# Optimization experiments

Hardware: AMD Instinct MI355X
Metric: run time of the kernel (lower is better)

The kernel has to match this reference:

```python
import jax, jax.numpy as jnp
import numpy as np

N_NODES = 100000
N_EDGES = 800000
IN_DIM = 128
HID = 128


def setup_inputs() -> dict:
    key = jax.random.key(0)
    ks = jax.random.split(key, 8)
    s = 0.05
    x = jax.random.normal(ks[0], (N_NODES, IN_DIM), jnp.float32)
    edge_index = jax.random.randint(ks[1], (2, N_EDGES), 0, N_NODES)
    return {
        "x": x,
        "edge_index": edge_index,
        "W1l": jax.random.normal(ks[2], (HID, IN_DIM), jnp.float32) * s,
        "b1l": jnp.zeros((HID,), jnp.float32),
        "W1r": jax.random.normal(ks[3], (HID, IN_DIM), jnp.float32) * s,
        "W2l": jax.random.normal(ks[4], (HID, HID), jnp.float32) * s,
        "b2l": jnp.zeros((HID,), jnp.float32),
        "W2r": jax.random.normal(ks[5], (HID, HID), jnp.float32) * s,
        "Wm1": jax.random.normal(ks[6], (HID, 2 * HID), jnp.float32) * s,
        "bm1": jnp.zeros((HID,), jnp.float32),
        "Wm2": jax.random.normal(ks[7], (1, HID), jnp.float32) * s,
        "bm2": jnp.zeros((1,), jnp.float32),
    }


def sage_conv(x, src, dst, Wl, bl, Wr):
    # PyG SAGEConv (mean aggr): out = lin_l(mean_{j in N(i)} x_j) + lin_r(x_i)
    msg = x[src]  # [E, d] gather of source features
    agg = jax.ops.segment_sum(msg, dst, num_segments=N_NODES)  # [N, d]
    deg = jax.ops.segment_sum(jnp.ones((src.shape[0],), x.dtype), dst, num_segments=N_NODES)
    agg = agg / jnp.maximum(deg, 1.0)[:, None]
    return agg @ Wl.T + bl + x @ Wr.T


def reference(x, edge_index, W1l, b1l, W1r, W2l, b2l, W2r, Wm1, bm1, Wm2, bm2):
    src, dst = edge_index[0], edge_index[1]
    h = jax.nn.relu(sage_conv(x, src, dst, W1l, b1l, W1r))  # dropout = identity (eval)
    h = jax.nn.relu(sage_conv(h, src, dst, W2l, b2l, W2r))
    ef = jnp.concatenate([h[src], h[dst]], axis=1)  # [E, 2*HID]
    hidden = jax.nn.relu(ef @ Wm1.T + bm1)  # [E, HID]
    logits = (hidden @ Wm2.T + bm2)[:, 0]  # [E]
    return jax.nn.sigmoid(logits)
```

## Files before the change

kernel.cpp:

```cpp
#include <hip/hip_runtime.h>
#include <math.h>

#define NN 100000
#define NE 800000
#define D 128

typedef __attribute__((ext_vector_type(8))) short bf16x8;
typedef __attribute__((ext_vector_type(8))) unsigned short u16x8;
typedef __attribute__((ext_vector_type(4))) float f32x4;
typedef __attribute__((ext_vector_type(2))) float f32x2;

constexpr size_t OFF_RS  = 0;
constexpr size_t OFF_CNT = 512 * 1024;
constexpr size_t OFF_CUR = 1024 * 1024;
constexpr size_t OFF_BS  = 1536 * 1024;
constexpr size_t OFF_WB  = 1552 * 1024;
constexpr size_t OFF_SRC = 2 * 1024 * 1024;
constexpr size_t OFF_EID = 6 * 1024 * 1024;
constexpr size_t OFF_V8  = 10 * 1024 * 1024;
constexpr size_t OFF_X8  = OFF_V8 + 13 * 1024 * 1024;
constexpr size_t OFF_H8  = OFF_X8 + 13 * 1024 * 1024;
constexpr size_t OFF_U8  = OFF_H8 + 13 * 1024 * 1024;

__device__ __forceinline__ unsigned short f2b(float f) {
    unsigned u = __builtin_bit_cast(unsigned, f);
    return (unsigned short)((u + 0x7FFFu + ((u >> 16) & 1u)) >> 16);
}
__device__ __forceinline__ float b2f(unsigned short h) {
    unsigned u = ((unsigned)h) << 16;
    return __builtin_bit_cast(float, u);
}

__global__ __launch_bounds__(256) void k_prep(const float* __restrict__ x,
                                              unsigned* __restrict__ x8w,
                                              const float* __restrict__ W1l,
                                              const float* __restrict__ W1r,
                                              const float* __restrict__ W2l,
                                              const float* __restrict__ W2r,
                                              const float* __restrict__ Wm1,
                                              unsigned short* __restrict__ wb,
                                              const int* __restrict__ dst,
                                              int* __restrict__ cnt) {
    int bid = blockIdx.x, tid = threadIdx.x;
    if (bid < 12500) {
        int i = bid * 256 + tid;
        float4 v = *(const float4*)&x[(size_t)i * 4];
        unsigned p = __builtin_amdgcn_cvt_pk_fp8_f32(v.x, v.y, 0u, false);
        p = __builtin_amdgcn_cvt_pk_fp8_f32(v.z, v.w, p, true);
        x8w[i] = p;
    } else if (bid < 12884) {
        int i = (bid - 12500) * 256 + tid;
        float v;
        if (i < 16384) v = W1l[i];
        else if (i < 32768) v = W1r[i - 16384];
        else if (i < 49152) v = W2l[i - 32768];
        else if (i < 65536) v = W2r[i - 49152];
        else v = Wm1[i - 65536];
        wb[i] = f2b(v);
    } else {
        int e = (bid - 12884) * 256 + tid;
        atomicAdd(&cnt[dst[e]], 1);
    }
}

__global__ __launch_bounds__(256) void k_scan1(const int* __restrict__ cnt,
                                               int* __restrict__ bsum) {
    int i = blockIdx.x * 256 + threadIdx.x;
    int v = (i < NN) ? cnt[i] : 0;
    #pragma unroll
    for (int o = 1; o < 64; o <<= 1) v += __shfl_xor(v, o);
    __shared__ int wsum[4];
    if ((threadIdx.x & 63) == 0) wsum[threadIdx.x >> 6] = v;
    __syncthreads();
    if (threadIdx.x == 0) bsum[blockIdx.x] = wsum[0] + wsum[1] + wsum[2] + wsum[3];
}

__global__ __launch_bounds__(512) void k_scan2(int* __restrict__ bsum, int nb) {
    __shared__ int s[512];
    int t = threadIdx.x;
    int v = (t < nb) ? bsum[t] : 0;
    s[t] = v;
    __syncthreads();
    for (int o = 1; o < 512; o <<= 1) {
        int u = (t >= o) ? s[t - o] : 0;
        __syncthreads();
        s[t] += u;
        __syncthreads();
    }
    if (t < nb) bsum[t] = s[t] - v;
}

__global__ __launch_bounds__(256) void k_scan3(const int* __restrict__ cnt,
                                               const int* __restrict__ bsum,
                                               int* __restrict__ rs,
                                               int* __restrict__ cur) {
    __shared__ int s[256];
    int t = threadIdx.x;
    int i = blockIdx.x * 256 + t;
    int v = (i < NN) ? cnt[i] : 0;
    s[t] = v;
    __syncthreads();
    for (int o = 1; o < 256; o <<= 1) {
        int u = (t >= o) ? s[t - o] : 0;
        __syncthreads();
        s[t] += u;
        __syncthreads();
    }
    int ex = s[t] - v + bsum[blockIdx.x];
    if (i < NN) { rs[i] = ex; cur[i] = ex; }
    if (i == NN - 1) rs[NN] = ex + v;
}

__global__ __launch_bounds__(256) void k_scatter_idx(const int* __restrict__ src,
                                                     const int* __restrict__ dst,
                                                     int* __restrict__ cur,
                                                     int* __restrict__ srcs,
                                                     int* __restrict__ eids) {
    int e = blockIdx.x * 256 + threadIdx.x;
    if (e < NE) {
        int pos = atomicAdd(&cur[dst[e]], 1);
        srcs[pos] = src[e];
        eids[pos] = e;
    }
}

#define UNPK8(acc, u) {                                               \
    f32x2 p0 = __builtin_amdgcn_cvt_pk_f32_fp8(u.x, false);           \
    f32x2 p1 = __builtin_amdgcn_cvt_pk_f32_fp8(u.x, true);            \
    f32x2 p2 = __builtin_amdgcn_cvt_pk_f32_fp8(u.y, false);           \
    f32x2 p3 = __builtin_amdgcn_cvt_pk_f32_fp8(u.y, true);            \
    acc[0] += p0.x; acc[1] += p0.y; acc[2] += p1.x; acc[3] += p1.y;   \
    acc[4] += p2.x; acc[5] += p2.y; acc[6] += p3.x; acc[7] += p3.y; }

__device__ __forceinline__ void gather_mean64(const unsigned char* __restrict__ feat8,
                                              const int* __restrict__ rs,
                                              const int* __restrict__ re,
                                              const int* __restrict__ srcs,
                                              int n0, unsigned short* agt) {
    const int tid = threadIdx.x;
    const int g = tid >> 4, q = tid & 15;
    #pragma unroll
    for (int half = 0; half < 2; ++half) {
        int r = half * 32 + g;
        int n = n0 + r;
        if (n > NN - 1) n = NN - 1;
        int b = rs[n], e = re[n];
        float a0[8] = {}, a1[8] = {}, a2[8] = {}, a3[8] = {};
        int j = b;
        for (; j + 7 < e; j += 8) {
            uint2 v0 = *(const uint2*)&feat8[(size_t)srcs[j]     * 128 + q * 8];
            uint2 v1 = *(const uint2*)&feat8[(size_t)srcs[j + 1] * 128 + q * 8];
            uint2 v2 = *(const uint2*)&feat8[(size_t)srcs[j + 2] * 128 + q * 8];
            uint2 v3 = *(const uint2*)&feat8[(size_t)srcs[j + 3] * 128 + q * 8];
            uint2 v4 = *(const uint2*)&feat8[(size_t)srcs[j + 4] * 128 + q * 8];
            uint2 v5 = *(const uint2*)&feat8[(size_t)srcs[j + 5] * 128 + q * 8];
            uint2 v6 = *(const uint2*)&feat8[(size_t)srcs[j + 6] * 128 + q * 8];
            uint2 v7 = *(const uint2*)&feat8[(size_t)srcs[j + 7] * 128 + q * 8];
            UNPK8(a0, v0); UNPK8(a1, v1); UNPK8(a2, v2); UNPK8(a3, v3);
            UNPK8(a0, v4); UNPK8(a1, v5); UNPK8(a2, v6); UNPK8(a3, v7);
        }
        for (; j + 3 < e; j += 4) {
            uint2 v0 = *(const uint2*)&feat8[(size_t)srcs[j]     * 128 + q * 8];
            uint2 v1 = *(const uint2*)&feat8[(size_t)srcs[j + 1] * 128 + q * 8];
            uint2 v2 = *(const uint2*)&feat8[(size_t)srcs[j + 2] * 128 + q * 8];
            uint2 v3 = *(const uint2*)&feat8[(size_t)srcs[j + 3] * 128 + q * 8];
            UNPK8(a0, v0); UNPK8(a1, v1); UNPK8(a2, v2); UNPK8(a3, v3);
        }
        for (; j < e; ++j) {
            uint2 v0 = *(const uint2*)&feat8[(size_t)srcs[j] * 128 + q * 8];
            UNPK8(a0, v0);
        }
        float inv = 1.0f / fmaxf((float)(e - b), 1.0f);
        u16x8 o;
        #pragma unroll
        for (int i = 0; i < 8; ++i) o[i] = f2b((a0[i] + a1[i] + a2[i] + a3[i]) * inv);
        *(u16x8*)&agt[r * 136 + q * 8] = o;
    }
}

__device__ __forceinline__ void stage_tile_fp8in(const unsigned char* __restrict__ src8,
                                                 int n0, unsigned short* t) {
    const int tid = threadIdx.x;
    int r = tid >> 3, q = tid & 7;
    int gr = n0 + r;
    if (gr > NN - 1) gr = NN - 1;
    uint4 v = *(const uint4*)&src8[(size_t)gr * 128 + q * 16];
    u16x8 o0, o1;
    f32x2 p;
    p = __builtin_amdgcn_cvt_pk_f32_fp8(v.x, false); o0[0] = f2b(p.x); o0[1] = f2b(p.y);
    p = __builtin_amdgcn_cvt_pk_f32_fp8(v.x, true);  o0[2] = f2b(p.x); o0[3] = f2b(p.y);
    p = __builtin_amdgcn_cvt_pk_f32_fp8(v.y, false); o0[4] = f2b(p.x); o0[5] = f2b(p.y);
    p = __builtin_amdgcn_cvt_pk_f32_fp8(v.y, true);  o0[6] = f2b(p.x); o0[7] = f2b(p.y);
    p = __builtin_amdgcn_cvt_pk_f32_fp8(v.z, false); o1[0] = f2b(p.x); o1[1] = f2b(p.y);
    p = __builtin_amdgcn_cvt_pk_f32_fp8(v.z, true);  o1[2] = f2b(p.x); o1[3] = f2b(p.y);
    p = __builtin_amdgcn_cvt_pk_f32_fp8(v.w, false); o1[4] = f2b(p.x); o1[5] = f2b(p.y);
    p = __builtin_amdgcn_cvt_pk_f32_fp8(v.w, true);  o1[6] = f2b(p.x); o1[7] = f2b(p.y);
    *(u16x8*)&t[r * 136 + q * 16]     = o0;
    *(u16x8*)&t[r * 136 + q * 16 + 8] = o1;
}

__device__ __forceinline__ void store_tile_fp8(const unsigned short* t,
                                               int n0, unsigned char* __restrict__ dst8) {
    const int tid = threadIdx.x;
    #pragma unroll
    for (int it = 0; it < 4; ++it) {
        int w = it * 512 + tid;
        int r = w >> 5, c4 = (w & 31) * 4;
        int gr = n0 + r;
        if (gr < NN) {
            unsigned p = __builtin_amdgcn_cvt_pk_fp8_f32(
                b2f(t[r * 136 + c4 + 0]), b2f(t[r * 136 + c4 + 1]), 0u, false);
            p = __builtin_amdgcn_cvt_pk_fp8_f32(
                b2f(t[r * 136 + c4 + 2]), b2f(t[r * 136 + c4 + 3]), p, true);
            *(unsigned*)&dst8[(size_t)gr * 128 + c4] = p;
        }
    }
}

__global__ __launch_bounds__(512) void k_aggconv1(const unsigned char* __restrict__ x8,
                                                  const int* __restrict__ rs,
                                                  const int* __restrict__ re,
                                                  const int* __restrict__ srcs,
                                                  const unsigned short* __restrict__ Wlb,
                                                  const unsigned short* __restrict__ Wrb,
                                                  const float* __restrict__ bias,
                                                  unsigned char* __restrict__ h8) {
    __shared__ unsigned short agt[64 * 136];
    __shared__ unsigned short sto[64 * 136];
    const int tid = threadIdx.x;
    const int n0 = blockIdx.x * 64;

    stage_tile_fp8in(x8, n0, sto);
    gather_mean64(x8, rs, re, srcs, n0, agt);
    __syncthreads();

    const int wv = tid >> 6, l = tid & 63;
    const int lrow = l & 15, lk = (l >> 4) * 8;
    f32x4 acc[4] = {};
    #pragma unroll
    for (int p = 0; p < 2; ++p) {
        const unsigned short* W  = p ? Wrb : Wlb;
        const unsigned short* At = p ? sto : agt;
        #pragma unroll
        for (int ks = 0; ks < 4; ++ks) {
            bf16x8 bfr = *(const bf16x8*)&W[(size_t)(wv * 16 + lrow) * D + ks * 32 + lk];
            #pragma unroll
            for (int mt = 0; mt < 4; ++mt) {
                bf16x8 af = *(const bf16x8*)&At[(mt * 16 + lrow) * 136 + ks * 32 + lk];
                acc[mt] = __builtin_amdgcn_mfma_f32_16x16x32_bf16(af, bfr, acc[mt], 0, 0, 0);
            }
        }
    }
    __syncthreads();
    const int orow = (l >> 4) * 4, ocol = l & 15;
    float bb = bias[wv * 16 + ocol];
    #pragma unroll
    for (int mt = 0; mt < 4; ++mt)
        #pragma unroll
        for (int j = 0; j < 4; ++j)
            sto[(mt * 16 + orow + j) * 136 + wv * 16 + ocol] =
                f2b(fmaxf(acc[mt][j] + bb, 0.0f));
    __syncthreads();
    store_tile_fp8(sto, n0, h8);
}

__global__ __launch_bounds__(512) void k_aggconv2uv(const unsigned char* __restrict__ h8,
                                                    const int* __restrict__ rs,
                                                    const int* __restrict__ re,
                                                    const int* __restrict__ srcs,
                                                    const unsigned short* __restrict__ Wlb,
                                                    const unsigned short* __restrict__ Wrb,
                                                    const float* __restrict__ bias,
                                                    const unsigned short* __restrict__ Wm1b,
                                                    const float* __restrict__ bm1,
                                                    unsigned char* __restrict__ U8,
                                                    unsigned char* __restrict__ V8) {
    __shared__ unsigned short agt[64 * 136];
    __shared__ unsigned short sto[64 * 136];
    const int tid = threadIdx.x;
    const int n0 = blockIdx.x * 64;

    stage_tile_fp8in(h8, n0, sto);
    gather_mean64(h8, rs, re, srcs, n0, agt);
    __syncthreads();

    const int wv = tid >> 6, l = tid & 63;
    const int lrow = l & 15, lk = (l >> 4) * 8;
    const int orow = (l >> 4) * 4, ocol = l & 15;

    f32x4 acc[4] = {};
    #pragma unroll
    for (int p = 0; p < 2; ++p) {
        const unsigned short* W  = p ? Wrb : Wlb;
        const unsigned short* At = p ? sto : agt;
        #pragma unroll
        for (int ks = 0; ks < 4; ++ks) {
            bf16x8 bfr = *(const bf16x8*)&W[(size_t)(wv * 16 + lrow) * D + ks * 32 + lk];
            #pragma unroll
            for (int mt = 0; mt < 4; ++mt) {
                bf16x8 af = *(const bf16x8*)&At[(mt * 16 + lrow) * 136 + ks * 32 + lk];
                acc[mt] = __builtin_amdgcn_mfma_f32_16x16x32_bf16(af, bfr, acc[mt], 0, 0, 0);
            }
        }
    }
    __syncthreads();
    {
        float bb = bias[wv * 16 + ocol];
        #pragma unroll
        for (int mt = 0; mt < 4; ++mt)
            #pragma unroll
            for (int j = 0; j < 4; ++j)
                agt[(mt * 16 + orow + j) * 136 + wv * 16 + ocol] =
                    f2b(fmaxf(acc[mt][j] + bb, 0.0f));
    }
    __syncthreads();

    f32x4 aU[4] = {}, aV[4] = {};
    #pragma unroll
    for (int ks = 0; ks < 4; ++ks) {
        bf16x8 bu = *(const bf16x8*)&Wm1b[(size_t)(wv * 16 + lrow) * 256 + ks * 32 + lk];
        bf16x8 bv = *(const bf16x8*)&Wm1b[(size_t)(wv * 16 + lrow) * 256 + 128 + ks * 32 + lk];
        #pragma unroll
        for (int mt = 0; mt < 4; ++mt) {
            bf16x8 af = *(const bf16x8*)&agt[(mt * 16 + lrow) * 136 + ks * 32 + lk];
            aU[mt] = __builtin_amdgcn_mfma_f32_16x16x32_bf16(af, bu, aU[mt], 0, 0, 0);
            aV[mt] = __builtin_amdgcn_mfma_f32_16x16x32_bf16(af, bv, aV[mt], 0, 0, 0);
        }
    }
    {
        float bb = bm1[wv * 16 + ocol];
        #pragma unroll
        for (int mt = 0; mt < 4; ++mt)
            #pragma unroll
            for (int j = 0; j < 4; ++j)
                sto[(mt * 16 + orow + j) * 136 + wv * 16 + ocol] = f2b(aU[mt][j] + bb);
    }
    __syncthreads();
    store_tile_fp8(sto, n0, U8);
    {
        #pragma unroll
        for (int mt = 0; mt < 4; ++mt)
            #pragma unroll
            for (int j = 0; j < 4; ++j)
                agt[(mt * 16 + orow + j) * 136 + wv * 16 + ocol] = f2b(aV[mt][j]);
    }
    __syncthreads();
    store_tile_fp8(agt, n0, V8);
}

__global__ __launch_bounds__(256) void k_edge2(const unsigned char* __restrict__ U8,
                                               const unsigned char* __restrict__ V8,
                                               const int* __restrict__ rs,
                                               const int* __restrict__ re,
                                               const int* __restrict__ srcs,
                                               const int* __restrict__ eids,
                                               const float* __restrict__ wm2,
                                               const float* __restrict__ bm2,
                                               float* __restrict__ out) {
    int t = blockIdx.x * 256 + threadIdx.x;
    int g = t >> 4, q = t & 15;
    if (g >= NN) return;
    int b = rs[g], e = re[g];
    if (b == e) return;
    uint2 vv = *(const uint2*)&V8[(size_t)g * 128 + q * 8];
    float vf[8], wf[8];
    {
        f32x2 p0 = __builtin_amdgcn_cvt_pk_f32_fp8(vv.x, false);
        f32x2 p1 = __builtin_amdgcn_cvt_pk_f32_fp8(vv.x, true);
        f32x2 p2 = __builtin_amdgcn_cvt_pk_f32_fp8(vv.y, false);
        f32x2 p3 = __builtin_amdgcn_cvt_pk_f32_fp8(vv.y, true);
        vf[0] = p0.x; vf[1] = p0.y; vf[2] = p1.x; vf[3] = p1.y;
        vf[4] = p2.x; vf[5] = p2.y; vf[6] = p3.x; vf[7] = p3.y;
    }
    float4 w0 = *(const float4*)&wm2[q * 8];
    float4 w1 = *(const float4*)&wm2[q * 8 + 4];
    wf[0] = w0.x; wf[1] = w0.y; wf[2] = w0.z; wf[3] = w0.w;
    wf[4] = w1.x; wf[5] = w1.y; wf[6] = w1.z; wf[7] = w1.w;
    const float bb = bm2[0];

#define EDOT(p, u) {                                                   \
    f32x2 q0 = __builtin_amdgcn_cvt_pk_f32_fp8(u.x, false);            \
    f32x2 q1 = __builtin_amdgcn_cvt_pk_f32_fp8(u.x, true);             \
    f32x2 q2 = __builtin_amdgcn_cvt_pk_f32_fp8(u.y, false);            \
    f32x2 q3 = __builtin_amdgcn_cvt_pk_f32_fp8(u.y, true);             \
    p += fmaxf(q0.x + vf[0], 0.0f) * wf[0] + fmaxf(q0.y + vf[1], 0.0f) * wf[1] \
       + fmaxf(q1.x + vf[2], 0.0f) * wf[2] + fmaxf(q1.y + vf[3], 0.0f) * wf[3] \
       + fmaxf(q2.x + vf[4], 0.0f) * wf[4] + fmaxf(q2.y + vf[5], 0.0f) * wf[5] \
       + fmaxf(q3.x + vf[6], 0.0f) * wf[6] + fmaxf(q3.y + vf[7], 0.0f) * wf[7]; }

    int j = b;
    for (; j + 7 < e; j += 8) {
        uint2 u0 = *(const uint2*)&U8[(size_t)srcs[j]     * 128 + q * 8];
        uint2 u1 = *(const uint2*)&U8[(size_t)srcs[j + 1] * 128 + q * 8];
        uint2 u2 = *(const uint2*)&U8[(size_t)srcs[j + 2] * 128 + q * 8];
        uint2 u3 = *(const uint2*)&U8[(size_t)srcs[j + 3] * 128 + q * 8];
        uint2 u4 = *(const uint2*)&U8[(size_t)srcs[j + 4] * 128 + q * 8];
        uint2 u5 = *(const uint2*)&U8[(size_t)srcs[j + 5] * 128 + q * 8];
        uint2 u6 = *(const uint2*)&U8[(size_t)srcs[j + 6] * 128 + q * 8];
        uint2 u7 = *(const uint2*)&U8[(size_t)srcs[j + 7] * 128 + q * 8];
        float p0 = 0.f, p1 = 0.f, p2 = 0.f, p3 = 0.f;
        float p4 = 0.f, p5 = 0.f, p6 = 0.f, p7 = 0.f;
        EDOT(p0, u0); EDOT(p1, u1); EDOT(p2, u2); EDOT(p3, u3);
        EDOT(p4, u4); EDOT(p5, u5); EDOT(p6, u6); EDOT(p7, u7);
        #pragma unroll
        for (int off = 1; off < 16; off <<= 1) {
            p0 += __shfl_xor(p0, off); p1 += __shfl_xor(p1, off);
            p2 += __shfl_xor(p2, off); p3 += __shfl_xor(p3, off);
            p4 += __shfl_xor(p4, off); p5 += __shfl_xor(p5, off);
            p6 += __shfl_xor(p6, off); p7 += __shfl_xor(p7, off);
        }
        if (q == 0) {
            out[eids[j]]     = 1.0f / (1.0f + expf(-(p0 + bb)));
            out[eids[j + 1]] = 1.0f / (1.0f + expf(-(p1 + bb)));
            out[eids[j + 2]] = 1.0f / (1.0f + expf(-(p2 + bb)));
            out[eids[j + 3]] = 1.0f / (1.0f + expf(-(p3 + bb)));
            out[eids[j + 4]] = 1.0f / (1.0f + expf(-(p4 + bb)));
            out[eids[j + 5]] = 1.0f / (1.0f + expf(-(p5 + bb)));
            out[eids[j + 6]] = 1.0f / (1.0f + expf(-(p6 + bb)));
            out[eids[j + 7]] = 1.0f / (1.0f + expf(-(p7 + bb)));
        }
    }
    for (; j + 3 < e; j += 4) {
        uint2 u0 = *(const uint2*)&U8[(size_t)srcs[j]     * 128 + q * 8];
        uint2 u1 = *(const uint2*)&U8[(size_t)srcs[j + 1] * 128 + q * 8];
        uint2 u2 = *(const uint2*)&U8[(size_t)srcs[j + 2] * 128 + q * 8];
        uint2 u3 = *(const uint2*)&U8[(size_t)srcs[j + 3] * 128 + q * 8];
        float p0 = 0.f, p1 = 0.f, p2 = 0.f, p3 = 0.f;
        EDOT(p0, u0); EDOT(p1, u1); EDOT(p2, u2); EDOT(p3, u3);
        #pragma unroll
        for (int off = 1; off < 16; off <<= 1) {
            p0 += __shfl_xor(p0, off); p1 += __shfl_xor(p1, off);
            p2 += __shfl_xor(p2, off); p3 += __shfl_xor(p3, off);
        }
        if (q == 0) {
            out[eids[j]]     = 1.0f / (1.0f + expf(-(p0 + bb)));
            out[eids[j + 1]] = 1.0f / (1.0f + expf(-(p1 + bb)));
            out[eids[j + 2]] = 1.0f / (1.0f + expf(-(p2 + bb)));
            out[eids[j + 3]] = 1.0f / (1.0f + expf(-(p3 + bb)));
        }
    }
    for (; j < e; ++j) {
        uint2 u0 = *(const uint2*)&U8[(size_t)srcs[j] * 128 + q * 8];
        float p0 = 0.f;
        EDOT(p0, u0);
        #pragma unroll
        for (int off = 1; off < 16; off <<= 1) p0 += __shfl_xor(p0, off);
        if (q == 0) out[eids[j]] = 1.0f / (1.0f + expf(-(p0 + bb)));
    }
}

extern "C" void kernel_launch(void* const* d_in, const int* in_sizes, int n_in,
                              void* d_out, int out_size, void* d_ws, size_t ws_size,
                              hipStream_t stream) {
    const float* x   = (const float*)d_in[0];
    const int*   ei  = (const int*)d_in[1];
    const int*   src = ei;
    const int*   dst = ei + NE;
    const float* W1l = (const float*)d_in[2];
    const float* b1l = (const float*)d_in[3];
    const float* W1r = (const float*)d_in[4];
    const float* W2l = (const float*)d_in[5];
    const float* b2l = (const float*)d_in[6];
    const float* W2r = (const float*)d_in[7];
    const float* Wm1 = (const float*)d_in[8];
    const float* bm1 = (const float*)d_in[9];
    const float* Wm2 = (const float*)d_in[10];
    const float* bm2 = (const float*)d_in[11];
    float* out = (float*)d_out;

    char* ws = (char*)d_ws;
    int* rs   = (int*)(ws + OFF_RS);
    int* cnt  = (int*)(ws + OFF_CNT);
    int* cur  = (int*)(ws + OFF_CUR);
    int* bsum = (int*)(ws + OFF_BS);
    unsigned short* wb = (unsigned short*)(ws + OFF_WB);
    int* srcs = (int*)(ws + OFF_SRC);
    int* eids = (int*)(ws + OFF_EID);
    unsigned char*  V8 = (unsigned char*)(ws + OFF_V8);
    unsigned char*  X8 = (unsigned char*)(ws + OFF_X8);
    unsigned char*  H8 = (unsigned char*)(ws + OFF_H8);
    unsigned char*  U8 = (unsigned char*)(ws + OFF_U8);

    unsigned short* W1lb = wb;
    unsigned short* W1rb = wb + 16384;
    unsigned short* W2lb = wb + 32768;
    unsigned short* W2rb = wb + 49152;
    unsigned short* Wm1b = wb + 65536;

    const int NB = 391;
    const int NB64 = (NN + 63) / 64;

    hipMemsetAsync(cnt, 0, NN * sizeof(int), stream);
    k_prep<<<12500 + 384 + 3125, 256, 0, stream>>>(x, (unsigned*)X8,
                                                   W1l, W1r, W2l, W2r, Wm1,
                                                   wb, dst, cnt);
    k_scan1<<<NB, 256, 0, stream>>>(cnt, bsum);
    k_scan2<<<1, 512, 0, stream>>>(bsum, NB);
    k_scan3<<<NB, 256, 0, stream>>>(cnt, bsum, rs, cur);
    k_scatter_idx<<<(NE + 255) / 256, 256, 0, stream>>>(src, dst, cur, srcs, eids);

    k_aggconv1<<<NB64, 512, 0, stream>>>(X8, rs, cur, srcs,
                                         W1lb, W1rb, b1l, H8);
    k_aggconv2uv<<<NB64, 512, 0, stream>>>(H8, rs, cur, srcs,
                                           W2lb, W2rb, b2l, Wm1b, bm1,
                                           U8, V8);
    k_edge2<<<(NN * 16 + 255) / 256, 256, 0, stream>>>(U8, V8, rs, cur, srcs, eids,
                                                       Wm2, bm2, out);
}
```

Baseline: 259.8 us.

## Interleave CSR src/eid into int2 and use packed bf16/f32x2 math

Merges the separate sorted source-index and edge-id arrays into one int2 array, so the scatter does one 8-byte store and the edge kernel gets both fields in a single load. Accumulation and the edge dot product now use packed f32x2 vector arithmetic. The software bf16 rounding is replaced by the hardware v_cvt_pk_bf16_f32 instruction. The gather kernels now read 8-byte entries where they only need the source field, which doubles index traffic there.

New measurement: 257.1 us. No clear change (-1.0%).

```diff
diff --git a/kernel.cpp b/kernel.cpp
--- a/kernel.cpp
+++ b/kernel.cpp
@@ -15,8 +15,7 @@
 constexpr size_t OFF_CUR = 1024 * 1024;
 constexpr size_t OFF_BS  = 1536 * 1024;
 constexpr size_t OFF_WB  = 1552 * 1024;
-constexpr size_t OFF_SRC = 2 * 1024 * 1024;
-constexpr size_t OFF_EID = 6 * 1024 * 1024;
+constexpr size_t OFF_SE  = 2 * 1024 * 1024;
 constexpr size_t OFF_V8  = 10 * 1024 * 1024;
 constexpr size_t OFF_X8  = OFF_V8 + 13 * 1024 * 1024;
 constexpr size_t OFF_H8  = OFF_X8 + 13 * 1024 * 1024;
@@ -29,6 +28,17 @@
 __device__ __forceinline__ float b2f(unsigned short h) {
     unsigned u = ((unsigned)h) << 16;
     return __builtin_bit_cast(float, u);
+}
+__device__ __forceinline__ unsigned pk_bf16(float lo, float hi) {
+    unsigned r;
+    asm("v_cvt_pk_bf16_f32 %0, %1, %2" : "=v"(r) : "v"(lo), "v"(hi));
+    return r;
+}
+__device__ __forceinline__ unsigned short f2b_fast(float f) {
+    return (unsigned short)pk_bf16(f, f);
+}
+__device__ __forceinline__ f32x2 relu2(f32x2 a) {
+    f32x2 r; r.x = fmaxf(a.x, 0.f); r.y = fmaxf(a.y, 0.f); return r;
 }
 
 __global__ __launch_bounds__(256) void k_prep(const float* __restrict__ x,
@@ -114,28 +124,24 @@
 __global__ __launch_bounds__(256) void k_scatter_idx(const int* __restrict__ src,
                                                      const int* __restrict__ dst,
                                                      int* __restrict__ cur,
-                                                     int* __restrict__ srcs,
-                                                     int* __restrict__ eids) {
+                                                     int2* __restrict__ se) {
     int e = blockIdx.x * 256 + threadIdx.x;
     if (e < NE) {
         int pos = atomicAdd(&cur[dst[e]], 1);
-        srcs[pos] = src[e];
-        eids[pos] = e;
-    }
-}
-
-#define UNPK8(acc, u) {                                               \
-    f32x2 p0 = __builtin_amdgcn_cvt_pk_f32_fp8(u.x, false);           \
-    f32x2 p1 = __builtin_amdgcn_cvt_pk_f32_fp8(u.x, true);            \
-    f32x2 p2 = __builtin_amdgcn_cvt_pk_f32_fp8(u.y, false);           \
-    f32x2 p3 = __builtin_amdgcn_cvt_pk_f32_fp8(u.y, true);            \
-    acc[0] += p0.x; acc[1] += p0.y; acc[2] += p1.x; acc[3] += p1.y;   \
-    acc[4] += p2.x; acc[5] += p2.y; acc[6] += p3.x; acc[7] += p3.y; }
+        se[pos] = make_int2(src[e], e);
+    }
+}
+
+#define UNPK8v(acc, u) {                                              \
+    acc[0] += __builtin_amdgcn_cvt_pk_f32_fp8(u.x, false);            \
+    acc[1] += __builtin_amdgcn_cvt_pk_f32_fp8(u.x, true);             \
+    acc[2] += __builtin_amdgcn_cvt_pk_f32_fp8(u.y, false);            \
+    acc[3] += __builtin_amdgcn_cvt_pk_f32_fp8(u.y, true); }
 
 __device__ __forceinline__ void gather_mean64(const unsigned char* __restrict__ feat8,
                                               const int* __restrict__ rs,
                                               const int* __restrict__ re,
-                                              const int* __restrict__ srcs,
+                                              const int2* __restrict__ se,
                                               int n0, unsigned short* agt) {
     const int tid = threadIdx.x;
     const int g = tid >> 4, q = tid & 15;
@@ -145,36 +151,43 @@
         int n = n0 + r;
         if (n > NN - 1) n = NN - 1;
         int b = rs[n], e = re[n];
-        float a0[8] = {}, a1[8] = {}, a2[8] = {}, a3[8] = {};
+        f32x2 a0[4] = {}, a1[4] = {}, a2[4] = {}, a3[4] = {};
         int j = b;
         for (; j + 7 < e; j += 8) {
-            uint2 v0 = *(const uint2*)&feat8[(size_t)srcs[j]     * 128 + q * 8];
-            uint2 v1 = *(const uint2*)&feat8[(size_t)srcs[j + 1] * 128 + q * 8];
-            uint2 v2 = *(const uint2*)&feat8[(size_t)srcs[j + 2] * 128 + q * 8];
-            uint2 v3 = *(const uint2*)&feat8[(size_t)srcs[j + 3] * 128 + q * 8];
-            uint2 v4 = *(const uint2*)&feat8[(size_t)srcs[j + 4] * 128 + q * 8];
-            uint2 v5 = *(const uint2*)&feat8[(size_t)srcs[j + 5] * 128 + q * 8];
-            uint2 v6 = *(const uint2*)&feat8[(size_t)srcs[j + 6] * 128 + q * 8];
-            uint2 v7 = *(const uint2*)&feat8[(size_t)srcs[j + 7] * 128 + q * 8];
-            UNPK8(a0, v0); UNPK8(a1, v1); UNPK8(a2, v2); UNPK8(a3, v3);
-            UNPK8(a0, v4); UNPK8(a1, v5); UNPK8(a2, v6); UNPK8(a3, v7);
+            uint2 v0 = *(const uint2*)&feat8[(size_t)se[j].x     * 128 + q * 8];
+            uint2 v1 = *(const uint2*)&feat8[(size_t)se[j + 1].x * 128 + q * 8];
+            uint2 v2 = *(const uint2*)&feat8[(size_t)se[j + 2].x * 128 + q * 8];
+            uint2 v3 = *(const uint2*)&feat8[(size_t)se[j + 3].x * 128 + q * 8];
+            uint2 v4 = *(const uint2*)&feat8[(size_t)se[j + 4].x * 128 + q * 8];
+            uint2 v5 = *(const uint2*)&feat8[(size_t)se[j + 5].x * 128 + q * 8];
+            uint2 v6 = *(const uint2*)&feat8[(size_t)se[j + 6].x * 128 + q * 8];
+            uint2 v7 = *(const uint2*)&feat8[(size_t)se[j + 7].x * 128 + q * 8];
+            UNPK8v(a0, v0); UNPK8v(a1, v1); UNPK8v(a2, v2); UNPK8v(a3, v3);
+            UNPK8v(a0, v4); UNPK8v(a1, v5); UNPK8v(a2, v6); UNPK8v(a3, v7);
         }
         for (; j + 3 < e; j += 4) {
-            uint2 v0 = *(const uint2*)&feat8[(size_t)srcs[j]     * 128 + q * 8];
-            uint2 v1 = *(const uint2*)&feat8[(size_t)srcs[j + 1] * 128 + q * 8];
-            uint2 v2 = *(const uint2*)&feat8[(size_t)srcs[j + 2] * 128 + q * 8];
-            uint2 v3 = *(const uint2*)&feat8[(size_t)srcs[j + 3] * 128 + q * 8];
-            UNPK8(a0, v0); UNPK8(a1, v1); UNPK8(a2, v2); UNPK8(a3, v3);
+            uint2 v0 = *(const uint2*)&feat8[(size_t)se[j].x     * 128 + q * 8];
+            uint2 v1 = *(const uint2*)&feat8[(size_t)se[j + 1].x * 128 + q * 8];
+            uint2 v2 = *(const uint2*)&feat8[(size_t)se[j + 2].x * 128 + q * 8];
+            uint2 v3 = *(const uint2*)&feat8[(size_t)se[j + 3].x * 128 + q * 8];
+            UNPK8v(a0, v0); UNPK8v(a1, v1); UNPK8v(a2, v2); UNPK8v(a3, v3);
         }
         for (; j < e; ++j) {
-            uint2 v0 = *(const uint2*)&feat8[(size_t)srcs[j] * 128 + q * 8];
-            UNPK8(a0, v0);
+            uint2 v0 = *(const uint2*)&feat8[(size_t)se[j].x * 128 + q * 8];
+            UNPK8v(a0, v0);
         }
         float inv = 1.0f / fmaxf((float)(e - b), 1.0f);
-        u16x8 o;
-        #pragma unroll
-        for (int i = 0; i < 8; ++i) o[i] = f2b((a0[i] + a1[i] + a2[i] + a3[i]) * inv);
-        *(u16x8*)&agt[r * 136 + q * 8] = o;
+        f32x2 iv; iv.x = inv; iv.y = inv;
+        f32x2 s0 = (a0[0] + a1[0] + a2[0] + a3[0]) * iv;
+        f32x2 s1 = (a0[1] + a1[1] + a2[1] + a3[1]) * iv;
+        f32x2 s2 = (a0[2] + a1[2] + a2[2] + a3[2]) * iv;
+        f32x2 s3 = (a0[3] + a1[3] + a2[3] + a3[3]) * iv;
+        uint4 o;
+        o.x = pk_bf16(s0.x, s0.y);
+        o.y = pk_bf16(s1.x, s1.y);
+        o.z = pk_bf16(s2.x, s2.y);
+        o.w = pk_bf16(s3.x, s3.y);
+        *(uint4*)&agt[r * 136 + q * 8] = o;
     }
 }
 
@@ -185,18 +198,22 @@
     int gr = n0 + r;
     if (gr > NN - 1) gr = NN - 1;
     uint4 v = *(const uint4*)&src8[(size_t)gr * 128 + q * 16];
-    u16x8 o0, o1;
-    f32x2 p;
-    p = __builtin_amdgcn_cvt_pk_f32_fp8(v.x, false); o0[0] = f2b(p.x); o0[1] = f2b(p.y);
-    p = __builtin_amdgcn_cvt_pk_f32_fp8(v.x, true);  o0[2] = f2b(p.x); o0[3] = f2b(p.y);
-    p = __builtin_amdgcn_cvt_pk_f32_fp8(v.y, false); o0[4] = f2b(p.x); o0[5] = f2b(p.y);
-    p = __builtin_amdgcn_cvt_pk_f32_fp8(v.y, true);  o0[6] = f2b(p.x); o0[7] = f2b(p.y);
-    p = __builtin_amdgcn_cvt_pk_f32_fp8(v.z, false); o1[0] = f2b(p.x); o1[1] = f2b(p.y);
-    p = __builtin_amdgcn_cvt_pk_f32_fp8(v.z, true);  o1[2] = f2b(p.x); o1[3] = f2b(p.y);
-    p = __builtin_amdgcn_cvt_pk_f32_fp8(v.w, false); o1[4] = f2b(p.x); o1[5] = f2b(p.y);
-    p = __builtin_amdgcn_cvt_pk_f32_fp8(v.w, true);  o1[6] = f2b(p.x); o1[7] = f2b(p.y);
-    *(u16x8*)&t[r * 136 + q * 16]     = o0;
-    *(u16x8*)&t[r * 136 + q * 16 + 8] = o1;
+    f32x2 p0 = __builtin_amdgcn_cvt_pk_f32_fp8(v.x, false);
+    f32x2 p1 = __builtin_amdgcn_cvt_pk_f32_fp8(v.x, true);
+    f32x2 p2 = __builtin_amdgcn_cvt_pk_f32_fp8(v.y, false);
+    f32x2 p3 = __builtin_amdgcn_cvt_pk_f32_fp8(v.y, true);
+    uint4 o0;
+    o0.x = pk_bf16(p0.x, p0.y); o0.y = pk_bf16(p1.x, p1.y);
+    o0.z = pk_bf16(p2.x, p2.y); o0.w = pk_bf16(p3.x, p3.y);
+    f32x2 p4 = __builtin_amdgcn_cvt_pk_f32_fp8(v.z, false);
+    f32x2 p5 = __builtin_amdgcn_cvt_pk_f32_fp8(v.z, true);
+    f32x2 p6 = __builtin_amdgcn_cvt_pk_f32_fp8(v.w, false);
+    f32x2 p7 = __builtin_amdgcn_cvt_pk_f32_fp8(v.w, true);
+    uint4 o1;
+    o1.x = pk_bf16(p4.x, p4.y); o1.y = pk_bf16(p5.x, p5.y);
+    o1.z = pk_bf16(p6.x, p6.y); o1.w = pk_bf16(p7.x, p7.y);
+    *(uint4*)&t[r * 136 + q * 16]     = o0;
+    *(uint4*)&t[r * 136 + q * 16 + 8] = o1;
 }
 
 __device__ __forceinline__ void store_tile_fp8(const unsigned short* t,
@@ -220,7 +237,7 @@
 __global__ __launch_bounds__(512) void k_aggconv1(const unsigned char* __restrict__ x8,
                                                   const int* __restrict__ rs,
                                                   const int* __restrict__ re,
-                                                  const int* __restrict__ srcs,
+                                                  const int2* __restrict__ se,
                                                   const unsigned short* __restrict__ Wlb,
                                                   const unsigned short* __restrict__ Wrb,
                                                   const float* __restrict__ bias,
@@ -231,7 +248,7 @@
     const int n0 = blockIdx.x * 64;
 
     stage_tile_fp8in(x8, n0, sto);
-    gather_mean64(x8, rs, re, srcs, n0, agt);
+    gather_mean64(x8, rs, re, se, n0, agt);
     __syncthreads();
 
     const int wv = tid >> 6, l = tid & 63;
@@ -259,7 +276,7 @@
         #pragma unroll
         for (int j = 0; j < 4; ++j)
             sto[(mt * 16 + orow + j) * 136 + wv * 16 + ocol] =
-                f2b(fmaxf(acc[mt][j] + bb, 0.0f));
+                f2b_fast(fmaxf(acc[mt][j] + bb, 0.0f));
     __syncthreads();
     store_tile_fp8(sto, n0, h8);
 }
@@ -267,7 +284,7 @@
 __global__ __launch_bounds__(512) void k_aggconv2uv(const unsigned char* __restrict__ h8,
                                                     const int* __restrict__ rs,
                                                     const int* __restrict__ re,
-                                                    const int* __restrict__ srcs,
+                                                    const int2* __restrict__ se,
                                                     const unsigned short* __restrict__ Wlb,
                                                     const unsigned short* __restrict__ Wrb,
                                                     const float* __restrict__ bias,
@@ -281,7 +298,7 @@
     const int n0 = blockIdx.x * 64;
 
     stage_tile_fp8in(h8, n0, sto);
-    gather_mean64(h8, rs, re, srcs, n0, agt);
+    gather_mean64(h8, rs, re, se, n0, agt);
     __syncthreads();
 
     const int wv = tid >> 6, l = tid & 63;
@@ -311,7 +328,7 @@
             #pragma unroll
             for (int j = 0; j < 4; ++j)
                 agt[(mt * 16 + orow + j) * 136 + wv * 16 + ocol] =
-                    f2b(fmaxf(acc[mt][j] + bb, 0.0f));
+                    f2b_fast(fmaxf(acc[mt][j] + bb, 0.0f));
     }
     __syncthreads();
 
@@ -333,7 +350,7 @@
         for (int mt = 0; mt < 4; ++mt)
             #pragma unroll
             for (int j = 0; j < 4; ++j)
-                sto[(mt * 16 + orow + j) * 136 + wv * 16 + ocol] = f2b(aU[mt][j] + bb);
+                sto[(mt * 16 + orow + j) * 136 + wv * 16 + ocol] = f2b_fast(aU[mt][j] + bb);
     }
     __syncthreads();
     store_tile_fp8(sto, n0, U8);
@@ -342,7 +359,7 @@
         for (int mt = 0; mt < 4; ++mt)
             #pragma unroll
             for (int j = 0; j < 4; ++j)
-                agt[(mt * 16 + orow + j) * 136 + wv * 16 + ocol] = f2b(aV[mt][j]);
+                agt[(mt * 16 + orow + j) * 136 + wv * 16 + ocol] = f2b_fast(aV[mt][j]);
     }
     __syncthreads();
     store_tile_fp8(agt, n0, V8);
@@ -352,8 +369,7 @@
                                                const unsigned char* __restrict__ V8,
                                                const int* __restrict__ rs,
                                                const int* __restrict__ re,
-                                               const int* __restrict__ srcs,
-                                               const int* __restrict__ eids,
+                                               const int2* __restrict__ se,
                                                const float* __restrict__ wm2,
                                                const float* __restrict__ bm2,
                                                float* __restrict__ out) {
@@ -363,45 +379,42 @@
     int b = rs[g], e = re[g];
     if (b == e) return;
     uint2 vv = *(const uint2*)&V8[(size_t)g * 128 + q * 8];
-    float vf[8], wf[8];
-    {
-        f32x2 p0 = __builtin_amdgcn_cvt_pk_f32_fp8(vv.x, false);
-        f32x2 p1 = __builtin_amdgcn_cvt_pk_f32_fp8(vv.x, true);
-        f32x2 p2 = __builtin_amdgcn_cvt_pk_f32_fp8(vv.y, false);
-        f32x2 p3 = __builtin_amdgcn_cvt_pk_f32_fp8(vv.y, true);
-        vf[0] = p0.x; vf[1] = p0.y; vf[2] = p1.x; vf[3] = p1.y;
-        vf[4] = p2.x; vf[5] = p2.y; vf[6] = p3.x; vf[7] = p3.y;
-    }
+    f32x2 vf2[4];
+    vf2[0] = __builtin_amdgcn_cvt_pk_f32_fp8(vv.x, false);
+    vf2[1] = __builtin_amdgcn_cvt_pk_f32_fp8(vv.x, true);
+    vf2[2] = __builtin_amdgcn_cvt_pk_f32_fp8(vv.y, false);
+    vf2[3] = __builtin_amdgcn_cvt_pk_f32_fp8(vv.y, true);
     float4 w0 = *(const float4*)&wm2[q * 8];
     float4 w1 = *(const float4*)&wm2[q * 8 + 4];
-    wf[0] = w0.x; wf[1] = w0.y; wf[2] = w0.z; wf[3] = w0.w;
-    wf[4] = w1.x; wf[5] = w1.y; wf[6] = w1.z; wf[7] = w1.w;
+    f32x2 wf2[4];
+    wf2[0].x = w0.x; wf2[0].y = w0.y; wf2[1].x = w0.z; wf2[1].y = w0.w;
+    wf2[2].x = w1.x; wf2[2].y = w1.y; wf2[3].x = w1.z; wf2[3].y = w1.w;
     const float bb = bm2[0];
 
-#define EDOT(p, u) {                                                   \
-    f32x2 q0 = __builtin_amdgcn_cvt_pk_f32_fp8(u.x, false);            \
-    f32x2 q1 = __builtin_amdgcn_cvt_pk_f32_fp8(u.x, true);             \
-    f32x2 q2 = __builtin_amdgcn_cvt_pk_f32_fp8(u.y, false);            \
-    f32x2 q3 = __builtin_amdgcn_cvt_pk_f32_fp8(u.y, true);             \
-    p += fmaxf(q0.x + vf[0], 0.0f) * wf[0] + fmaxf(q0.y + vf[1], 0.0f) * wf[1] \
-       + fmaxf(q1.x + vf[2], 0.0f) * wf[2] + fmaxf(q1.y + vf[3], 0.0f) * wf[3] \
-       + fmaxf(q2.x + vf[4], 0.0f) * wf[4] + fmaxf(q2.y + vf[5], 0.0f) * wf[5] \
-       + fmaxf(q3.x + vf[6], 0.0f) * wf[6] + fmaxf(q3.y + vf[7], 0.0f) * wf[7]; }
+#define EDOTv(p2, u) {                                                   \
+    f32x2 t0 = relu2(__builtin_amdgcn_cvt_pk_f32_fp8(u.x, false) + vf2[0]); \
+    f32x2 t1 = relu2(__builtin_amdgcn_cvt_pk_f32_fp8(u.x, true)  + vf2[1]); \
+    f32x2 t2 = relu2(__builtin_amdgcn_cvt_pk_f32_fp8(u.y, false) + vf2[2]); \
+    f32x2 t3 = relu2(__builtin_amdgcn_cvt_pk_f32_fp8(u.y, true)  + vf2[3]); \
+    p2 += t0 * wf2[0] + t1 * wf2[1] + t2 * wf2[2] + t3 * wf2[3]; }
 
     int j = b;
     for (; j + 7 < e; j += 8) {
-        uint2 u0 = *(const uint2*)&U8[(size_t)srcs[j]     * 128 + q * 8];
-        uint2 u1 = *(const uint2*)&U8[(size_t)srcs[j + 1] * 128 + q * 8];
-        uint2 u2 = *(const uint2*)&U8[(size_t)srcs[j + 2] * 128 + q * 8];
-        uint2 u3 = *(const uint2*)&U8[(size_t)srcs[j + 3] * 128 + q * 8];
-        uint2 u4 = *(const uint2*)&U8[(size_t)srcs[j + 4] * 128 + q * 8];
-        uint2 u5 = *(const uint2*)&U8[(size_t)srcs[j + 5] * 128 + q * 8];
-        uint2 u6 = *(const uint2*)&U8[(size_t)srcs[j + 6] * 128 + q * 8];
-        uint2 u7 = *(const uint2*)&U8[(size_t)srcs[j + 7] * 128 + q * 8];
-        float p0 = 0.f, p1 = 0.f, p2 = 0.f, p3 = 0.f;
-        float p4 = 0.f, p5 = 0.f, p6 = 0.f, p7 = 0.f;
-        EDOT(p0, u0); EDOT(p1, u1); EDOT(p2, u2); EDOT(p3, u3);
-        EDOT(p4, u4); EDOT(p5, u5); EDOT(p6, u6); EDOT(p7, u7);
+        int2 s0 = se[j],     s1 = se[j + 1], s2 = se[j + 2], s3 = se[j + 3];
+        int2 s4 = se[j + 4], s5 = se[j + 5], s6 = se[j + 6], s7 = se[j + 7];
+        uint2 u0 = *(const uint2*)&U8[(size_t)s0.x * 128 + q * 8];
+        uint2 u1 = *(const uint2*)&U8[(size_t)s1.x * 128 + q * 8];
+        uint2 u2 = *(const uint2*)&U8[(size_t)s2.x * 128 + q * 8];
+        uint2 u3 = *(const uint2*)&U8[(size_t)s3.x * 128 + q * 8];
+        uint2 u4 = *(const uint2*)&U8[(size_t)s4.x * 128 + q * 8];
+        uint2 u5 = *(const uint2*)&U8[(size_t)s5.x * 128 + q * 8];
+        uint2 u6 = *(const uint2*)&U8[(size_t)s6.x * 128 + q * 8];
+        uint2 u7 = *(const uint2*)&U8[(size_t)s7.x * 128 + q * 8];
+        f32x2 q0 = {}, q1 = {}, q2 = {}, q3 = {}, q4 = {}, q5 = {}, q6 = {}, q7 = {};
+        EDOTv(q0, u0); EDOTv(q1, u1); EDOTv(q2, u2); EDOTv(q3, u3);
+        EDOTv(q4, u4); EDOTv(q5, u5); EDOTv(q6, u6); EDOTv(q7, u7);
+        float p0 = q0.x + q0.y, p1 = q1.x + q1.y, p2 = q2.x + q2.y, p3 = q3.x + q3.y;
+        float p4 = q4.x + q4.y, p5 = q5.x + q5.y, p6 = q6.x + q6.y, p7 = q7.x + q7.y;
         #pragma unroll
         for (int off = 1; off < 16; off <<= 1) {
             p0 += __shfl_xor(p0, off); p1 += __shfl_xor(p1, off);
@@ -410,42 +423,46 @@
             p6 += __shfl_xor(p6, off); p7 += __shfl_xor(p7, off);
         }
         if (q == 0) {
-            out[eids[j]]     = 1.0f / (1.0f + expf(-(p0 + bb)));
-            out[eids[j + 1]] = 1.0f / (1.0f + expf(-(p1 + bb)));
-            out[eids[j + 2]] = 1.0f / (1.0f + expf(-(p2 + bb)));
-            out[eids[j + 3]] = 1.0f / (1.0f + expf(-(p3 + bb)));
-            out[eids[j + 4]] = 1.0f / (1.0f + expf(-(p4 + bb)));
-            out[eids[j + 5]] = 1.0f / (1.0f + expf(-(p5 + bb)));
-            out[eids[j + 6]] = 1.0f / (1.0f + expf(-(p6 + bb)));
-            out[eids[j + 7]] = 1.0f / (1.0f + expf(-(p7 + bb)));
+            out[s0.y] = 1.0f / (1.0f + expf(-(p0 + bb)));
+            out[s1.y] = 1.0f / (1.0f + expf(-(p1 + bb)));
+            out[s2.y] = 1.0f / (1.0f + expf(-(p2 + bb)));
+            out[s3.y] = 1.0f / (1.0f + expf(-(p3 + bb)));
+            out[s4.y] = 1.0f / (1.0f + expf(-(p4 + bb)));
+            out[s5.y] = 1.0f / (1.0f + expf(-(p5 + bb)));
+            out[s6.y] = 1.0f / (1.0f + expf(-(p6 + bb)));
+            out[s7.y] = 1.0f / (1.0f + expf(-(p7 + bb)));
         }
     }
     for (; j + 3 < e; j += 4) {
-        uint2 u0 = *(const uint2*)&U8[(size_t)srcs[j]     * 128 + q * 8];
-        uint2 u1 = *(const uint2*)&U8[(size_t)srcs[j + 1] * 128 + q * 8];
-        uint2 u2 = *(const uint2*)&U8[(size_t)srcs[j + 2] * 128 + q * 8];
-        uint2 u3 = *(const uint2*)&U8[(size_t)srcs[j + 3] * 128 + q * 8];
-        float p0 = 0.f, p1 = 0.f, p2 = 0.f, p3 = 0.f;
-        EDOT(p0, u0); EDOT(p1, u1); EDOT(p2, u2); EDOT(p3, u3);
+        int2 s0 = se[j], s1 = se[j + 1], s2 = se[j + 2], s3 = se[j + 3];
+        uint2 u0 = *(const uint2*)&U8[(size_t)s0.x * 128 + q * 8];
+        uint2 u1 = *(const uint2*)&U8[(size_t)s1.x * 128 + q * 8];
+        uint2 u2 = *(const uint2*)&U8[(size_t)s2.x * 128 + q * 8];
+        uint2 u3 = *(const uint2*)&U8[(size_t)s3.x * 128 + q * 8];
+        f32x2 q0 = {}, q1 = {}, q2 = {}, q3 = {};
+        EDOTv(q0, u0); EDOTv(q1, u1); EDOTv(q2, u2); EDOTv(q3, u3);
+        float p0 = q0.x + q0.y, p1 = q1.x + q1.y, p2 = q2.x + q2.y, p3 = q3.x + q3.y;
         #pragma unroll
         for (int off = 1; off < 16; off <<= 1) {
             p0 += __shfl_xor(p0, off); p1 += __shfl_xor(p1, off);
             p2 += __shfl_xor(p2, off); p3 += __shfl_xor(p3, off);
         }
         if (q == 0) {
-            out[eids[j]]     = 1.0f / (1.0f + expf(-(p0 + bb)));
-            out[eids[j + 1]] = 1.0f / (1.0f + expf(-(p1 + bb)));
-            out[eids[j + 2]] = 1.0f / (1.0f + expf(-(p2 + bb)));
-            out[eids[j + 3]] = 1.0f / (1.0f + expf(-(p3 + bb)));
+            out[s0.y] = 1.0f / (1.0f + expf(-(p0 + bb)));
+            out[s1.y] = 1.0f / (1.0f + expf(-(p1 + bb)));
+            out[s2.y] = 1.0f / (1.0f + expf(-(p2 + bb)));
+            out[s3.y] = 1.0f / (1.0f + expf(-(p3 + bb)));
         }
     }
     for (; j < e; ++j) {
-        uint2 u0 = *(const uint2*)&U8[(size_t)srcs[j] * 128 + q * 8];
-        float p0 = 0.f;
-        EDOT(p0, u0);
+        int2 s0 = se[j];
+        uint2 u0 = *(const uint2*)&U8[(size_t)s0.x * 128 + q * 8];
+        f32x2 q0 = {};
+        EDOTv(q0, u0);
+        float p0 = q0.x + q0.y;
         #pragma unroll
         for (int off = 1; off < 16; off <<= 1) p0 += __shfl_xor(p0, off);
-        if (q == 0) out[eids[j]] = 1.0f / (1.0f + expf(-(p0 + bb)));
+        if (q == 0) out[s0.y] = 1.0f / (1.0f + expf(-(p0 + bb)));
     }
 }
 
@@ -474,8 +491,7 @@
     int* cur  = (int*)(ws + OFF_CUR);
     int* bsum = (int*)(ws + OFF_BS);
     unsigned short* wb = (unsigned short*)(ws + OFF_WB);
-    int* srcs = (int*)(ws + OFF_SRC);
-    int* eids = (int*)(ws + OFF_EID);
+    int2* se  = (int2*)(ws + OFF_SE);
     unsigned char*  V8 = (unsigned char*)(ws + OFF_V8);
     unsigned char*  X8 = (unsigned char*)(ws + OFF_X8);
     unsigned char*  H8 = (unsigned char*)(ws + OFF_H8);
@@ -497,13 +513,13 @@
     k_scan1<<<NB, 256, 0, stream>>>(cnt, bsum);
     k_scan2<<<1, 512, 0, stream>>>(bsum, NB);
     k_scan3<<<NB, 256, 0, stream>>>(cnt, bsum, rs, cur);
-    k_scatter_idx<<<(NE + 255) / 256, 256, 0, stream>>>(src, dst, cur, srcs, eids);
-
-    k_aggconv1<<<NB64, 512, 0, stream>>>(X8, rs, cur, srcs,
+    k_scatter_idx<<<(NE + 255) / 256, 256, 0, stream>>>(src, dst, cur, se);
+
+    k_aggconv1<<<NB64, 512, 0, stream>>>(X8, rs, cur, se,
                                          W1lb, W1rb, b1l, H8);
-    k_aggconv2uv<<<NB64, 512, 0, stream>>>(H8, rs, cur, srcs,
+    k_aggconv2uv<<<NB64, 512, 0, stream>>>(H8, rs, cur, se,
                                            W2lb, W2rb, b2l, Wm1b, bm1,
                                            U8, V8);
-    k_edge2<<<(NN * 16 + 255) / 256, 256, 0, stream>>>(U8, V8, rs, cur, srcs, eids,
+    k_edge2<<<(NN * 16 + 255) / 256, 256, 0, stream>>>(U8, V8, rs, cur, se,
                                                        Wm2, bm2, out);
 }
```
